# Optimization experiments

Hardware: AMD Instinct MI355X
Metric: run time of the kernel (lower is better)

Reference implementation:

```python
import jax, jax.numpy as jnp
import numpy as np

B, S, D = 4, 2048, 1024
H = 16
HD = D // H
DFF = 4096
MAX_REL = 32
EPS = 1e-5


def _rms_norm(x, w):
    rms = jnp.sqrt(jnp.mean(x * x, axis=-1, keepdims=True) + EPS)
    return x / rms * w


def setup_inputs() -> dict:
    key = jax.random.key(0)
    ks = jax.random.split(key, 16)
    sc = 0.02
    d = {
        "x": jax.random.normal(ks[0], (B, S, D), dtype=jnp.float32),
        "g1": jnp.ones((D,), dtype=jnp.float32),
        "g2": jnp.ones((D,), dtype=jnp.float32),
        "wq": jax.random.normal(ks[1], (D, D), dtype=jnp.float32) * sc,
        "bq": jnp.zeros((D,), dtype=jnp.float32),
        "wk": jax.random.normal(ks[2], (D, D), dtype=jnp.float32) * sc,
        "bk": jnp.zeros((D,), dtype=jnp.float32),
        "wv": jax.random.normal(ks[3], (D, D), dtype=jnp.float32) * sc,
        "bv": jnp.zeros((D,), dtype=jnp.float32),
        "wo": jax.random.normal(ks[4], (D, D), dtype=jnp.float32) * sc,
        "bo": jnp.zeros((D,), dtype=jnp.float32),
        "rel_pos": jax.random.normal(ks[5], (H, 2 * MAX_REL + 1), dtype=jnp.float32),
        "w1": jax.random.normal(ks[6], (D, DFF), dtype=jnp.float32) * sc,
        "b1": jnp.zeros((DFF,), dtype=jnp.float32),
        "w2": jax.random.normal(ks[7], (DFF, D), dtype=jnp.float32) * sc,
        "b2": jnp.zeros((D,), dtype=jnp.float32),
    }
    return d


def reference(x, g1, g2, wq, bq, wk, bk, wv, bv, wo, bo, rel_pos, w1, b1, w2, b2):
    b, s, d = x.shape
    # --- multi-head attention with relative-position bias ---
    q = (x @ wq + bq).reshape(b, s, H, HD).transpose(0, 2, 1, 3)  # [B,H,S,HD]
    k = (x @ wk + bk).reshape(b, s, H, HD).transpose(0, 2, 1, 3)
    v = (x @ wv + bv).reshape(b, s, H, HD).transpose(0, 2, 1, 3)
    scores = jnp.einsum("bhqd,bhkd->bhqk", q, k) / jnp.sqrt(jnp.float32(HD))
    # relative position bias: gather from (H, 2*MAX_REL+1) table
    pos = jnp.arange(s)
    rel = pos[None, :] - pos[:, None]                # [S,S]
    idx = jnp.clip(rel, -MAX_REL, MAX_REL) + MAX_REL  # [S,S]
    bias = rel_pos[:, idx]                            # [H,S,S]
    scores = scores + bias[None]
    attn = jax.nn.softmax(scores, axis=-1)
    out = jnp.einsum("bhqk,bhkd->bhqd", attn, v)
    out = out.transpose(0, 2, 1, 3).reshape(b, s, d)
    attn_out = out @ wo + bo
    # residual + RMSNorm
    x = _rms_norm(attn_out + x, g1)
    # --- feed-forward (exact GELU) ---
    h = jax.nn.gelu(x @ w1 + b1, approximate=False)
    ff = h @ w2 + b2
    x = _rms_norm(ff + x, g2)
    return x
```

## Files before the change

kernel.cpp:

```cpp
#include <hip/hip_runtime.h>

#define B_ 4
#define S_ 2048
#define D_ 1024
#define H_ 16
#define HD_ 64
#define DFF_ 4096
#define MR_ 32
#define M_ (B_*S_)

typedef unsigned short u16;
typedef __attribute__((ext_vector_type(8))) short bf16x8;
typedef __attribute__((ext_vector_type(4))) float f32x4;

#define MFMA16 __builtin_amdgcn_mfma_f32_16x16x32_bf16
#define A_CONST 0.18033688011112f
#define LOG2E_ 1.44269504088896f

__device__ __forceinline__ u16 f2b(float f) {
  unsigned u = __builtin_bit_cast(unsigned, f);
  u = u + 0x7FFFu + ((u >> 16) & 1u);
  return (u16)(u >> 16);
}
__device__ __forceinline__ float b2f(u16 h) {
  unsigned u = ((unsigned)h) << 16;
  return __builtin_bit_cast(float, u);
}
__device__ __forceinline__ float exp2_fast(float x) {
  float r;
  asm("v_exp_f32 %0, %1" : "=v"(r) : "v"(x));
  return r;
}
__device__ __forceinline__ unsigned cvtpk(float lo, float hi) {
  unsigned r;
  asm("v_cvt_pk_bf16_f32 %0, %1, %2" : "=v"(r) : "v"(lo), "v"(hi));
  return r;
}
__device__ __forceinline__ int med3i(int a, int b, int c) {
  int r;
  asm("v_med3_i32 %0, %1, %2, %3" : "=v"(r) : "v"(a), "v"(b), "v"(c));
  return r;
}
__device__ __forceinline__ float gelu_t(float v) {
  float v2 = v * v;
  float z  = v * fmaf(v2, 0.1029394f, 2.3021171f);
  float e  = exp2_fast(z);
  float r;
  asm("v_rcp_f32 %0, %1" : "=v"(r) : "v"(e + 1.0f));
  return v - v * r;
}
__device__ __forceinline__ void gl_lds16(const void* g, void* l) {
  __builtin_amdgcn_global_load_lds(
      (const __attribute__((address_space(1))) void*)g,
      (__attribute__((address_space(3))) void*)l, 16, 0, 0);
}

#define SWZ(r) ((((((r)>>3)&1)<<2) ^ ((r)&7)) << 4)
#define SWZ64(r) ((((r)>>1)&3) << 4)

__global__ __launch_bounds__(256) void prep_kernel(
    const float* __restrict__ x, u16* __restrict__ xb,
    const float* __restrict__ wq, const float* __restrict__ wk,
    const float* __restrict__ wv, const float* __restrict__ wo,
    const float* __restrict__ w1, const float* __restrict__ w2,
    u16* __restrict__ wqT, u16* __restrict__ wkT, u16* __restrict__ wvT,
    u16* __restrict__ woT, u16* __restrict__ w1T, u16* __restrict__ w2T)
{
  int bid = blockIdx.x;
  const int tid = threadIdx.x;
  if (bid < 8192) {
    int i = bid * 256 + tid;
    float4 v = ((const float4*)x)[i];
    ushort4 o;
    o.x = f2b(v.x); o.y = f2b(v.y); o.z = f2b(v.z); o.w = f2b(v.w);
    ((ushort4*)xb)[i] = o;
    return;
  }
  bid -= 8192;
  const float* in; u16* out; int R, C, local;
  if (bid < 4096) {
    int m = bid >> 10;
    in  = m == 0 ? wq  : (m == 1 ? wk  : (m == 2 ? wv  : wo));
    out = m == 0 ? wqT : (m == 1 ? wkT : (m == 2 ? wvT : woT));
    R = 1024; C = 1024; local = bid & 1023;
  } else if (bid < 8192) {
    in = w1; out = w1T; R = 1024; C = 4096; local = bid - 4096;
  } else {
    in = w2; out = w2T; R = 4096; C = 1024; local = bid - 8192;
  }
  const int ctiles = C >> 5;
  const int c0 = (local % ctiles) * 32;
  const int r0 = (local / ctiles) * 32;
  const int xx = tid & 31, yy = tid >> 5;
  __shared__ float t[32][33];
#pragma unroll
  for (int i = 0; i < 4; ++i)
    t[yy + i*8][xx] = in[(long)(r0 + yy + i*8) * C + c0 + xx];
  __syncthreads();
#pragma unroll
  for (int i = 0; i < 4; ++i)
    out[(long)(c0 + yy + i*8) * R + r0 + xx] = f2b(t[xx][yy + i*8]);
}

__global__ __launch_bounds__(256) void vtrans_kernel(const u16* __restrict__ v,
                                                     u16* __restrict__ vT) {
  __shared__ u16 t[32][33];
  int bh = blockIdx.y; int b = bh >> 4, h = bh & 15;
  int s0 = (blockIdx.x >> 1) * 32;
  int d0 = (blockIdx.x & 1) * 32;
  int x = threadIdx.x, y = threadIdx.y;
#pragma unroll
  for (int i = 0; i < 4; ++i)
    t[y + i*8][x] = v[((long)(b*S_ + s0 + y + i*8)) * D_ + h*64 + d0 + x];
  __syncthreads();
#pragma unroll
  for (int i = 0; i < 4; ++i)
    vT[((long)((b*H_ + h)*HD_ + d0 + y + i*8)) * S_ + s0 + x] = t[x][y + i*8];
}

template<int EPI, int WN>
__global__ __launch_bounds__(512, 2) void gemm10(
    const u16* __restrict__ A, const u16* __restrict__ BT,
    const float* __restrict__ bias0, const float* __restrict__ bias1,
    const float* __restrict__ bias2,
    u16* __restrict__ C0, u16* __restrict__ C1, u16* __restrict__ C2,
    int Ndim, int Kdim)
{
  constexpr int BM = (WN == 4) ? 128 : 256;
  constexpr int BN = WN * 64;
  constexpr int SLOT = (BM + BN) * 64;
  __shared__ char lds[3 * SLOT];
  const int tid = threadIdx.x;
  const int w = tid >> 6, lane = tid & 63;
  const int lr = lane & 15, lg = lane >> 4;
  const int wm = w / WN, wn = w % WN;

  const int nbx = Ndim / BN;
  const int cpx = gridDim.x >> 3;
  const int bid = blockIdx.x;
  const int swzb = (bid & 7) * cpx + (bid >> 3);
  const long blockM = (long)(swzb / nbx) * BM;
  const long blockN = (long)(swzb % nbx) * BN;

  const int srow = tid >> 2;
  const int scol = ((tid & 3) * 16) ^ SWZ64(srow);
  const u16* Ag  = A  + (blockM + srow) * (long)Kdim + (scol >> 1);
  const u16* Ag2 = Ag + (long)128 * Kdim;
  const u16* Bg  = BT + (blockN + srow) * (long)Kdim + (scol >> 1);
  const u16* Bg2 = Bg + (long)128 * Kdim;

  auto STAGE = [&](int slot, long ko) {
    char* base = &lds[slot * SLOT];
    gl_lds16(Ag + ko, base + w * 1024);
    if constexpr (WN == 2) gl_lds16(Ag2 + ko, base + 8192 + w * 1024);
    gl_lds16(Bg + ko, base + BM * 64 + w * 1024);
    if constexpr (WN == 4) gl_lds16(Bg2 + ko, base + BM * 64 + 8192 + w * 1024);
  };

  const int rsw = (lg * 16) ^ SWZ64(lr);
  int offA[4], offB[4];
#pragma unroll
  for (int mf = 0; mf < 4; ++mf) offA[mf] = (wm*64 + mf*16 + lr) * 64 + rsw;
#pragma unroll
  for (int nf = 0; nf < 4; ++nf) offB[nf] = BM*64 + (wn*64 + nf*16 + lr) * 64 + rsw;

  f32x4 acc[4][4] = {};
  const int NS = Kdim >> 5;

  STAGE(0, 0);
  STAGE(1, 32);
  asm volatile("s_waitcnt vmcnt(3)" ::: "memory");
  __builtin_amdgcn_s_barrier();

  int sl = 0, sl2 = 2;
  for (int t = 0; t < NS; ++t) {
    const char* s = &lds[sl * SLOT];
    bf16x8 af[4], bfr[4];
#pragma unroll
    for (int mf = 0; mf < 4; ++mf) af[mf] = *(const bf16x8*)(s + offA[mf]);
#pragma unroll
    for (int nf = 0; nf < 4; ++nf) bfr[nf] = *(const bf16x8*)(s + offB[nf]);
    if (t + 2 < NS) {
      STAGE(sl2, (long)(t + 2) * 32);
      asm volatile("s_waitcnt vmcnt(3)" ::: "memory");
    } else if (t == NS - 2) {
      asm volatile("s_waitcnt vmcnt(0)" ::: "memory");
    }
    __builtin_amdgcn_s_barrier();
    __builtin_amdgcn_s_setprio(1);
#pragma unroll
    for (int mf = 0; mf < 4; ++mf)
#pragma unroll
      for (int nf = 0; nf < 4; ++nf)
        acc[mf][nf] = MFMA16(bfr[nf], af[mf], acc[mf][nf], 0, 0, 0);
    __builtin_amdgcn_s_setprio(0);
    sl  = (sl  == 2) ? 0 : sl  + 1;
    sl2 = (sl2 == 2) ? 0 : sl2 + 1;
  }

  const float* bsel = bias0;
  u16* osel = C0;
  long nstride = Ndim;
  long ncol0 = blockN;
  if (EPI == 3) {
    int mat = (int)(blockN >> 10);
    bsel = mat == 0 ? bias0 : (mat == 1 ? bias1 : bias2);
    osel = mat == 0 ? C0 : (mat == 1 ? C1 : C2);
    nstride = 1024;
    ncol0 = blockN & 1023;
  }
  constexpr int RB = BN * 2;
  char* const et = &lds[0];
  __syncthreads();
#pragma unroll
  for (int mf = 0; mf < 4; ++mf) {
    const int row = wm*64 + mf*16 + lr;
#pragma unroll
    for (int nf = 0; nf < 4; ++nf) {
      const int colu = wn*64 + nf*16 + lg*4;
      float4 bv = *(const float4*)&bsel[ncol0 + colu];
      float v0 = acc[mf][nf][0] + bv.x;
      float v1 = acc[mf][nf][1] + bv.y;
      float v2 = acc[mf][nf][2] + bv.z;
      float v3 = acc[mf][nf][3] + bv.w;
      if (EPI == 2) {
        v0 = gelu_t(v0); v1 = gelu_t(v1); v2 = gelu_t(v2); v3 = gelu_t(v3);
      }
      ushort4 st;
      st.x = f2b(v0); st.y = f2b(v1); st.z = f2b(v2); st.w = f2b(v3);
      *(ushort4*)(et + row*RB + ((colu*2) ^ ((row & 7) << 4))) = st;
    }
  }
  __syncthreads();
  constexpr int CHR  = RB / 16;
  constexpr int ITER = BM * CHR / 512;
#pragma unroll
  for (int i = 0; i < ITER; ++i) {
    const int idx = i*512 + tid;
    const int row = idx / CHR;
    const int cb  = (idx % CHR) * 16;
    uint4 val = *(const uint4*)(et + row*RB + (cb ^ ((row & 7) << 4)));
    *(uint4*)&osel[(blockM + row) * nstride + ncol0 + (cb >> 1)] = val;
  }
}

__device__ __forceinline__ void packp(const float* p, bf16x8* pfo) {
#pragma unroll
  for (int ks = 0; ks < 2; ++ks) {
    uint4 uu;
    uu.x = cvtpk(p[ks*4+0], p[ks*4+1]);
    uu.y = cvtpk(p[ks*4+2], p[ks*4+3]);
    uu.z = cvtpk(p[(ks+2)*4+0], p[(ks+2)*4+1]);
    uu.w = cvtpk(p[(ks+2)*4+2], p[(ks+2)*4+3]);
    pfo[ks] = __builtin_bit_cast(bf16x8, uu);
  }
}

__device__ __forceinline__ void sm_uni(const f32x4* s, float bu, bf16x8* pfo) {
  float p[16];
#pragma unroll
  for (int ni = 0; ni < 4; ++ni)
#pragma unroll
    for (int j = 0; j < 4; ++j)
      p[ni*4+j] = exp2_fast(fmaf(s[ni][j], A_CONST, bu));
  packp(p, pfo);
}

__device__ __forceinline__ void sm_slow(const f32x4* s, const float* relb,
                                        int rbase, bf16x8* pfo) {
  float p[16];
#pragma unroll
  for (int ni = 0; ni < 4; ++ni) {
    const int koff = (ni&1)*32 + (ni>>1)*4;
#pragma unroll
    for (int j = 0; j < 4; ++j) {
      int idx = med3i(rbase + koff + j + MR_, 0, 2*MR_);
      p[ni*4+j] = exp2_fast(fmaf(s[ni][j], A_CONST, relb[idx]));
    }
  }
  packp(p, pfo);
}

__global__ __launch_bounds__(256, 2) void attn7_kernel(
    const u16* __restrict__ q, const u16* __restrict__ k,
    const u16* __restrict__ vT, const float* __restrict__ rel_pos,
    u16* __restrict__ ao)
{
  __shared__ u16 SM[16384];
  __shared__ float relb[2*MR_ + 1];

  const int tid = threadIdx.x;
  const int w = tid >> 6, lane = tid & 63;
  const int lr = lane & 15, lg = lane >> 4;
  const int qt = blockIdx.x, bh = blockIdx.y;
  const int b = bh >> 4, h = bh & 15;
  const int q0 = qt * 256;
  const int qlo = q0 + w*64;

  if (tid < 2*MR_ + 1) relb[tid] = rel_pos[h * (2*MR_ + 1) + tid] * LOG2E_;

  const int srow0 = w*8 + (lane >> 3);
  const int srow1 = 32 + srow0;
  const int scb   = (lane & 7) * 16;
  const int col0  = scb ^ SWZ(srow0);
  const int col1  = scb ^ SWZ(srow1);

  const long qkbase = ((long)(b*S_)) * D_ + h*64;
  const long vbase  = ((long)((b*H_ + h) * HD_)) * S_;

  {
    const u16* qg = q + qkbase + (long)q0 * D_;
#pragma unroll
    for (int c = 0; c < 8; ++c)
      gl_lds16(qg + (long)(c*32 + srow0)*D_ + (col0 >> 1), &SM[(c*32 + w*8)*64]);
  }
  __syncthreads();
  bf16x8 qf[4][2];
#pragma unroll
  for (int qi = 0; qi < 4; ++qi)
#pragma unroll
    for (int ks = 0; ks < 2; ++ks) {
      int row = w*64 + qi*16 + lr;
      qf[qi][ks] = *(const bf16x8*)((const char*)&SM[0] + row*128 + ((ks*64 + lg*16) ^ SWZ(row)));
    }
  const float bHI = relb[2*MR_];
  const float bLO = relb[0];
  __syncthreads();

  int offK0[4], offV0[4];
#pragma unroll
  for (int ni = 0; ni < 4; ++ni) {
    int kr = (ni&1)*32 + (lr>>2)*8 + (ni>>1)*4 + (lr&3);
    int vr = ni*16 + lr;
    offK0[ni] = kr*128 + ((lg*16) ^ SWZ(kr));
    offV0[ni] = vr*128 + ((lg*16) ^ SWZ(vr));
  }

  const u16* kp0 = k  + qkbase + (long)srow0*D_ + (col0 >> 1);
  const u16* kp1 = k  + qkbase + (long)srow1*D_ + (col1 >> 1);
  const u16* vp0 = vT + vbase  + (long)srow0*S_ + (col0 >> 1);
  const u16* vp1 = vT + vbase  + (long)srow1*S_ + (col1 >> 1);
  u16* kb_w0 = &SM[(w*8)*64];
  u16* kb_w1 = &SM[(32 + w*8)*64];
  u16* vb_w0 = &SM[8192 + (w*8)*64];
  u16* vb_w1 = &SM[8192 + (32 + w*8)*64];

  bf16x8 onesf;
#pragma unroll
  for (int i = 0; i < 8; ++i) onesf[i] = (short)0x3F80;

  f32x4 acco[4][4] = {};
  f32x4 accl[4] = {};

  gl_lds16(kp0, kb_w0);
  gl_lds16(kp1, kb_w1);
  gl_lds16(vp0, vb_w0);
  gl_lds16(vp1, vb_w1);

  const long kstep = (long)64 * D_;
  const int NT = S_ / 64;
  for (int t = 0; t < NT; ++t) {
    const int cur = t & 1;
    __syncthreads();
    if (t + 1 < NT) {
      int bufo = (cur ^ 1) * 4096;
      gl_lds16(kp0 + (long)(t+1)*kstep, kb_w0 + bufo);
      gl_lds16(kp1 + (long)(t+1)*kstep, kb_w1 + bufo);
      gl_lds16(vp0 + (t+1)*64, vb_w0 + bufo);
      gl_lds16(vp1 + (t+1)*64, vb_w1 + bufo);
    }
    const char* Kb = (const char*)&SM[cur * 4096];
    const char* Vb = (const char*)&SM[8192 + cur * 4096];
    const int k0 = t * 64;

    f32x4 sc[4][4] = {};
#pragma unroll
    for (int ks = 0; ks < 2; ++ks)
#pragma unroll
      for (int ni = 0; ni < 4; ++ni) {
        bf16x8 kf = *(const bf16x8*)(Kb + (offK0[ni] ^ (ks*64)));
#pragma unroll
        for (int qi = 0; qi < 4; ++qi)
          sc[qi][ni] = MFMA16(kf, qf[qi][ks], sc[qi][ni], 0, 0, 0);
      }

    bf16x8 pf[4][2];
    bool hi_u = (k0 - (qlo + 63)) >= MR_;
    bool lo_u = (qlo - (k0 + 63)) >= MR_;
    if (hi_u || lo_u) {
      float bu = hi_u ? bHI : bLO;
#pragma unroll
      for (int qi = 0; qi < 4; ++qi) sm_uni(sc[qi], bu, pf[qi]);
    } else {
      int rb0 = k0 + lg*8 - (qlo + lr);
#pragma unroll
      for (int qi = 0; qi < 4; ++qi) sm_slow(sc[qi], relb, rb0 - qi*16, pf[qi]);
    }

#pragma unroll
    for (int ks = 0; ks < 2; ++ks) {
#pragma unroll
      for (int ni = 0; ni < 4; ++ni) {
        bf16x8 vf = *(const bf16x8*)(Vb + (offV0[ni] ^ (ks*64)));
#pragma unroll
        for (int qi = 0; qi < 4; ++qi)
          acco[qi][ni] = MFMA16(vf, pf[qi][ks], acco[qi][ni], 0, 0, 0);
      }
#pragma unroll
      for (int qi = 0; qi < 4; ++qi)
        accl[qi] = MFMA16(onesf, pf[qi][ks], accl[qi], 0, 0, 0);
    }
  }

#pragma unroll
  for (int qi = 0; qi < 4; ++qi) {
    float inv = 1.0f / accl[qi][0];
    long orow = ((long)(b*S_ + qlo + qi*16 + lr)) * D_ + h*64;
#pragma unroll
    for (int ni = 0; ni < 4; ++ni) {
      ushort4 ov;
      ov.x = f2b(acco[qi][ni][0] * inv);
      ov.y = f2b(acco[qi][ni][1] * inv);
      ov.z = f2b(acco[qi][ni][2] * inv);
      ov.w = f2b(acco[qi][ni][3] * inv);
      *(ushort4*)(ao + orow + ni*16 + lg*4) = ov;
    }
  }
}

template<int ABF, int BBF>
__global__ __launch_bounds__(256) void rmsnorm_kernel(
    const void* __restrict__ a, const void* __restrict__ b,
    const float* __restrict__ g, float* __restrict__ outf,
    u16* __restrict__ outb)
{
  long row = blockIdx.x;
  int tid = threadIdx.x;
  float ya[4], yb[4], y[4];
  if (ABF) {
    ushort4 av = ((const ushort4*)a)[row*256 + tid];
    ya[0] = b2f(av.x); ya[1] = b2f(av.y); ya[2] = b2f(av.z); ya[3] = b2f(av.w);
  } else {
    float4 av = ((const float4*)a)[row*256 + tid];
    ya[0] = av.x; ya[1] = av.y; ya[2] = av.z; ya[3] = av.w;
  }
  if (BBF) {
    ushort4 bv = ((const ushort4*)b)[row*256 + tid];
    yb[0] = b2f(bv.x); yb[1] = b2f(bv.y); yb[2] = b2f(bv.z); yb[3] = b2f(bv.w);
  } else {
    float4 bv = ((const float4*)b)[row*256 + tid];
    yb[0] = bv.x; yb[1] = bv.y; yb[2] = bv.z; yb[3] = bv.w;
  }
  float ss = 0.f;
#pragma unroll
  for (int i = 0; i < 4; ++i) { y[i] = ya[i] + yb[i]; ss += y[i]*y[i]; }
#pragma unroll
  for (int m = 1; m < 64; m <<= 1) ss += __shfl_xor(ss, m);
  __shared__ float red[4];
  int w = tid >> 6, lane = tid & 63;
  if (lane == 0) red[w] = ss;
  __syncthreads();
  ss = red[0] + red[1] + red[2] + red[3];
  float rinv = rsqrtf(ss * (1.0f / D_) + 1e-5f);
  float4 gv = ((const float4*)g)[tid];
  float o[4] = { y[0]*rinv*gv.x, y[1]*rinv*gv.y, y[2]*rinv*gv.z, y[3]*rinv*gv.w };
  if (outf) {
    float4 of = { o[0], o[1], o[2], o[3] };
    ((float4*)outf)[row*256 + tid] = of;
  }
  if (outb) {
    ushort4 ob;
    ob.x = f2b(o[0]); ob.y = f2b(o[1]); ob.z = f2b(o[2]); ob.w = f2b(o[3]);
    ((ushort4*)outb)[row*256 + tid] = ob;
  }
}

extern "C" void kernel_launch(void* const* d_in, const int* in_sizes, int n_in,
                              void* d_out, int out_size, void* d_ws, size_t ws_size,
                              hipStream_t stream) {
  const float* x   = (const float*)d_in[0];
  const float* g1  = (const float*)d_in[1];
  const float* g2  = (const float*)d_in[2];
  const float* wq  = (const float*)d_in[3];
  const float* bq  = (const float*)d_in[4];
  const float* wk  = (const float*)d_in[5];
  const float* bk  = (const float*)d_in[6];
  const float* wv  = (const float*)d_in[7];
  const float* bv  = (const float*)d_in[8];
  const float* wo  = (const float*)d_in[9];
  const float* bo  = (const float*)d_in[10];
  const float* rel = (const float*)d_in[11];
  const float* w1  = (const float*)d_in[12];
  const float* b1  = (const float*)d_in[13];
  const float* w2  = (const float*)d_in[14];
  const float* b2  = (const float*)d_in[15];
  float* out = (float*)d_out;

  char* ws = (char*)d_ws;
  const size_t MB = 1024ull * 1024ull;
  u16* xb   = (u16*)(ws + 0);
  u16* wqT  = (u16*)(ws + 16*MB);
  u16* wkT  = (u16*)(ws + 18*MB);
  u16* wvT  = (u16*)(ws + 20*MB);
  u16* woT  = (u16*)(ws + 22*MB);
  u16* w1T  = (u16*)(ws + 24*MB);
  u16* w2T  = (u16*)(ws + 32*MB);
  u16* qb   = (u16*)(ws + 40*MB);
  u16* kb   = (u16*)(ws + 56*MB);
  u16* vb   = (u16*)(ws + 72*MB);
  u16* vTb  = (u16*)(ws + 88*MB);
  u16* aob  = (u16*)(ws + 104*MB);
  u16* prjb = (u16*)(ws + 120*MB);
  u16* x1b  = (u16*)(ws + 136*MB);
  u16* hb   = (u16*)(ws + 40*MB);
  u16* ffb  = (u16*)(ws + 120*MB);
  (void)ws_size; (void)in_sizes; (void)n_in; (void)out_size;

  prep_kernel<<<20480, 256, 0, stream>>>(
      x, xb, wq, wk, wv, wo, w1, w2, wqT, wkT, wvT, woT, w1T, w2T);

  gemm10<3,4><<<(3072/256)*(M_/128), 512, 0, stream>>>(
      xb, wqT, bq, bk, bv, qb, kb, vb, 3072, D_);

  vtrans_kernel<<<dim3((S_/32)*(HD_/32), B_*H_), dim3(32, 8), 0, stream>>>(vb, vTb);

  attn7_kernel<<<dim3(S_/256, B_*H_), 256, 0, stream>>>(qb, kb, vTb, rel, aob);

  gemm10<0,2><<<(D_/128)*(M_/256), 512, 0, stream>>>(
      aob, woT, bo, nullptr, nullptr, prjb, nullptr, nullptr, D_, D_);

  rmsnorm_kernel<1,1><<<M_, 256, 0, stream>>>(prjb, xb, g1, nullptr, x1b);

  gemm10<2,4><<<(DFF_/256)*(M_/128), 512, 0, stream>>>(
      x1b, w1T, b1, nullptr, nullptr, hb, nullptr, nullptr, DFF_, D_);

  gemm10<0,2><<<(D_/128)*(M_/256), 512, 0, stream>>>(
      hb, w2T, b2, nullptr, nullptr, ffb, nullptr, nullptr, D_, DFF_);

  rmsnorm_kernel<1,1><<<M_, 256, 0, stream>>>(ffb, x1b, g2, out, nullptr);
}
```

Before: 376.9 us.

## Fuse V transpose into QKV GEMM epilogue and residual adds into projection GEMMs

```diff
diff --git a/kernel.cpp b/kernel.cpp
--- a/kernel.cpp
+++ b/kernel.cpp
@@ -102,28 +102,13 @@
     out[(long)(c0 + yy + i*8) * R + r0 + xx] = f2b(t[xx][yy + i*8]);
 }
 
-__global__ __launch_bounds__(256) void vtrans_kernel(const u16* __restrict__ v,
-                                                     u16* __restrict__ vT) {
-  __shared__ u16 t[32][33];
-  int bh = blockIdx.y; int b = bh >> 4, h = bh & 15;
-  int s0 = (blockIdx.x >> 1) * 32;
-  int d0 = (blockIdx.x & 1) * 32;
-  int x = threadIdx.x, y = threadIdx.y;
-#pragma unroll
-  for (int i = 0; i < 4; ++i)
-    t[y + i*8][x] = v[((long)(b*S_ + s0 + y + i*8)) * D_ + h*64 + d0 + x];
-  __syncthreads();
-#pragma unroll
-  for (int i = 0; i < 4; ++i)
-    vT[((long)((b*H_ + h)*HD_ + d0 + y + i*8)) * S_ + s0 + x] = t[x][y + i*8];
-}
-
 template<int EPI, int WN>
 __global__ __launch_bounds__(512, 2) void gemm10(
     const u16* __restrict__ A, const u16* __restrict__ BT,
     const float* __restrict__ bias0, const float* __restrict__ bias1,
     const float* __restrict__ bias2,
     u16* __restrict__ C0, u16* __restrict__ C1, u16* __restrict__ C2,
+    const u16* __restrict__ res,
     int Ndim, int Kdim)
 {
   constexpr int BM = (WN == 4) ? 128 : 256;
@@ -202,16 +187,38 @@
   u16* osel = C0;
   long nstride = Ndim;
   long ncol0 = blockN;
+  int mat = 0;
   if (EPI == 3) {
-    int mat = (int)(blockN >> 10);
+    mat = (int)(blockN >> 10);
     bsel = mat == 0 ? bias0 : (mat == 1 ? bias1 : bias2);
-    osel = mat == 0 ? C0 : (mat == 1 ? C1 : C2);
+    osel = mat == 0 ? C0 : C1;
     nstride = 1024;
     ncol0 = blockN & 1023;
   }
+  __syncthreads();
+
+  if (EPI == 3 && mat == 2) {
+#pragma unroll
+    for (int mf = 0; mf < 4; ++mf) {
+      const int row = wm*64 + mf*16 + lr;
+      const long m = blockM + row;
+      const long b = m >> 11, sg = m & 2047;
+#pragma unroll
+      for (int nf = 0; nf < 4; ++nf) {
+#pragma unroll
+        for (int j = 0; j < 4; ++j) {
+          const long colg = ncol0 + wn*64 + nf*16 + lg*4 + j;
+          float v = acc[mf][nf][j] + bsel[colg];
+          const long h = colg >> 6, hd = colg & 63;
+          C2[((b*16 + h)*64 + hd)*2048 + sg] = f2b(v);
+        }
+      }
+    }
+    return;
+  }
+
   constexpr int RB = BN * 2;
   char* const et = &lds[0];
-  __syncthreads();
 #pragma unroll
   for (int mf = 0; mf < 4; ++mf) {
     const int row = wm*64 + mf*16 + lr;
@@ -225,6 +232,10 @@
       float v3 = acc[mf][nf][3] + bv.w;
       if (EPI == 2) {
         v0 = gelu_t(v0); v1 = gelu_t(v1); v2 = gelu_t(v2); v3 = gelu_t(v3);
+      }
+      if (EPI == 4) {
+        ushort4 rv = *(const ushort4*)&res[(blockM + row) * 1024 + ncol0 + colu];
+        v0 += b2f(rv.x); v1 += b2f(rv.y); v2 += b2f(rv.z); v3 += b2f(rv.w);
       }
       ushort4 st;
       st.x = f2b(v0); st.y = f2b(v1); st.z = f2b(v2); st.w = f2b(v3);
@@ -428,32 +439,18 @@
   }
 }
 
-template<int ABF, int BBF>
-__global__ __launch_bounds__(256) void rmsnorm_kernel(
-    const void* __restrict__ a, const void* __restrict__ b,
-    const float* __restrict__ g, float* __restrict__ outf,
-    u16* __restrict__ outb)
+template<int OUTF>
+__global__ __launch_bounds__(256) void rms1_kernel(
+    const u16* __restrict__ a, const float* __restrict__ g,
+    float* __restrict__ outf, u16* __restrict__ outb)
 {
   long row = blockIdx.x;
   int tid = threadIdx.x;
-  float ya[4], yb[4], y[4];
-  if (ABF) {
-    ushort4 av = ((const ushort4*)a)[row*256 + tid];
-    ya[0] = b2f(av.x); ya[1] = b2f(av.y); ya[2] = b2f(av.z); ya[3] = b2f(av.w);
-  } else {
-    float4 av = ((const float4*)a)[row*256 + tid];
-    ya[0] = av.x; ya[1] = av.y; ya[2] = av.z; ya[3] = av.w;
-  }
-  if (BBF) {
-    ushort4 bv = ((const ushort4*)b)[row*256 + tid];
-    yb[0] = b2f(bv.x); yb[1] = b2f(bv.y); yb[2] = b2f(bv.z); yb[3] = b2f(bv.w);
-  } else {
-    float4 bv = ((const float4*)b)[row*256 + tid];
-    yb[0] = bv.x; yb[1] = bv.y; yb[2] = bv.z; yb[3] = bv.w;
-  }
+  ushort4 av = ((const ushort4*)a)[row*256 + tid];
+  float y[4] = { b2f(av.x), b2f(av.y), b2f(av.z), b2f(av.w) };
   float ss = 0.f;
 #pragma unroll
-  for (int i = 0; i < 4; ++i) { y[i] = ya[i] + yb[i]; ss += y[i]*y[i]; }
+  for (int i = 0; i < 4; ++i) ss += y[i]*y[i];
 #pragma unroll
   for (int m = 1; m < 64; m <<= 1) ss += __shfl_xor(ss, m);
   __shared__ float red[4];
@@ -464,11 +461,10 @@
   float rinv = rsqrtf(ss * (1.0f / D_) + 1e-5f);
   float4 gv = ((const float4*)g)[tid];
   float o[4] = { y[0]*rinv*gv.x, y[1]*rinv*gv.y, y[2]*rinv*gv.z, y[3]*rinv*gv.w };
-  if (outf) {
+  if (OUTF) {
     float4 of = { o[0], o[1], o[2], o[3] };
     ((float4*)outf)[row*256 + tid] = of;
-  }
-  if (outb) {
+  } else {
     ushort4 ob;
     ob.x = f2b(o[0]); ob.y = f2b(o[1]); ob.z = f2b(o[2]); ob.w = f2b(o[3]);
     ((ushort4*)outb)[row*256 + tid] = ob;
@@ -507,7 +503,6 @@
   u16* w2T  = (u16*)(ws + 32*MB);
   u16* qb   = (u16*)(ws + 40*MB);
   u16* kb   = (u16*)(ws + 56*MB);
-  u16* vb   = (u16*)(ws + 72*MB);
   u16* vTb  = (u16*)(ws + 88*MB);
   u16* aob  = (u16*)(ws + 104*MB);
   u16* prjb = (u16*)(ws + 120*MB);
@@ -520,22 +515,20 @@
       x, xb, wq, wk, wv, wo, w1, w2, wqT, wkT, wvT, woT, w1T, w2T);
 
   gemm10<3,4><<<(3072/256)*(M_/128), 512, 0, stream>>>(
-      xb, wqT, bq, bk, bv, qb, kb, vb, 3072, D_);
-
-  vtrans_kernel<<<dim3((S_/32)*(HD_/32), B_*H_), dim3(32, 8), 0, stream>>>(vb, vTb);
+      xb, wqT, bq, bk, bv, qb, kb, vTb, nullptr, 3072, D_);
 
   attn7_kernel<<<dim3(S_/256, B_*H_), 256, 0, stream>>>(qb, kb, vTb, rel, aob);
 
-  gemm10<0,2><<<(D_/128)*(M_/256), 512, 0, stream>>>(
-      aob, woT, bo, nullptr, nullptr, prjb, nullptr, nullptr, D_, D_);
-
-  rmsnorm_kernel<1,1><<<M_, 256, 0, stream>>>(prjb, xb, g1, nullptr, x1b);
+  gemm10<4,2><<<(D_/128)*(M_/256), 512, 0, stream>>>(
+      aob, woT, bo, nullptr, nullptr, prjb, nullptr, nullptr, xb, D_, D_);
+
+  rms1_kernel<0><<<M_, 256, 0, stream>>>(prjb, g1, nullptr, x1b);
 
   gemm10<2,4><<<(DFF_/256)*(M_/128), 512, 0, stream>>>(
-      x1b, w1T, b1, nullptr, nullptr, hb, nullptr, nullptr, DFF_, D_);
-
-  gemm10<0,2><<<(D_/128)*(M_/256), 512, 0, stream>>>(
-      hb, w2T, b2, nullptr, nullptr, ffb, nullptr, nullptr, D_, DFF_);
-
-  rmsnorm_kernel<1,1><<<M_, 256, 0, stream>>>(ffb, x1b, g2, out, nullptr);
-}
+      x1b, w1T, b1, nullptr, nullptr, hb, nullptr, nullptr, nullptr, DFF_, D_);
+
+  gemm10<4,2><<<(D_/128)*(M_/256), 512, 0, stream>>>(
+      hb, w2T, b2, nullptr, nullptr, ffb, nullptr, nullptr, x1b, D_, DFF_);
+
+  rms1_kernel<1><<<M_, 256, 0, stream>>>(ffb, g2, out, nullptr);
+}
```

Result: no change. 374.1 us (-0.8%).
